# Kernel optimization log

Measured on AMD Instinct MI355X. Metric: run time of the kernel, lower is better.

Reference implementation:

```python
import jax, jax.numpy as jnp
import numpy as np

N = 100000   # nodes (in_ch)
D = 128      # emb_ch
E = 1600000  # nonzeros in A_hat
RATE = 0.1   # dropout rate


def setup_inputs() -> dict:
    key = jax.random.key(0)
    k1, k2, k3, k4, k5, k6 = jax.random.split(key, 6)
    x = jnp.arange(N, dtype=jnp.int64) if jax.config.jax_enable_x64 else jnp.arange(N, dtype=jnp.int32)
    rows = jax.random.randint(k1, (E,), 0, N)
    cols = jax.random.randint(k2, (E,), 0, N)
    A_vals = jax.random.uniform(k3, (E,), dtype=jnp.float32)
    # xavier_uniform for [N, D]: bound = sqrt(6/(N+D))
    bound = float(np.sqrt(6.0 / (N + D)))
    emb_weight = jax.random.uniform(k4, (N, D), jnp.float32, -bound, bound)
    u1 = jax.random.uniform(k5, (N, D), dtype=jnp.float32)
    u2 = jax.random.uniform(k6, (N, D), dtype=jnp.float32)
    return {"x": x, "rows": rows, "cols": cols, "A_vals": A_vals,
            "emb_weight": emb_weight, "u1": u1, "u2": u2}


def _dropout(h, u):
    keep = (u >= RATE).astype(h.dtype)
    return h * keep / (1.0 - RATE)


def _spmm(rows, cols, vals, h):
    # out[i] = sum_{e: rows[e]==i} vals[e] * h[cols[e]]  -- COO SpMM
    msgs = vals[:, None] * h[cols]  # [E, D]
    return jax.ops.segment_sum(msgs, rows, num_segments=N)


def reference(x, rows, cols, A_vals, emb_weight, u1, u2):
    h0 = emb_weight[x]                       # embedding lookup [N, D]
    h1 = _spmm(rows, cols, A_vals, _dropout(h0, u1))
    h2 = _spmm(rows, cols, A_vals, _dropout(h1, u2))
    return (h0 + h1 + h2) / 3.0
```

## Files before the change

kernel.cpp:

```cpp
#include <hip/hip_runtime.h>
#include <hip/hip_fp16.h>

#define DD 128
#define SCAN_CHUNK 1024
#define G_ROWS 32
#define G_STAGE 1024
#define NCOPY 8

typedef float          f32x4 __attribute__((ext_vector_type(4)));
typedef unsigned int   u32x4 __attribute__((ext_vector_type(4)));
typedef unsigned int   u32x2 __attribute__((ext_vector_type(2)));
typedef unsigned short u16x8 __attribute__((ext_vector_type(8)));

struct __align__(8) Edge { int c; float v; };

__device__ __forceinline__ unsigned short f2h(float f) {
    return __half_as_ushort(__float2half(f));
}
__device__ __forceinline__ float2 up2(unsigned int u) {
    __half2 h = *reinterpret_cast<const __half2*>(&u);
    return __half22float2(h);
}

template <typename T>
__device__ __forceinline__ T ldnt(const T* p) { return __builtin_nontemporal_load(p); }
template <typename T>
__device__ __forceinline__ void stnt(T* p, T v) { __builtin_nontemporal_store(v, p); }

__global__ __launch_bounds__(256) void k_g1hist(const float* __restrict__ emb,
                                                const float* __restrict__ u1,
                                                ushort* __restrict__ g1,
                                                const int* __restrict__ rows,
                                                int* __restrict__ cnt8,
                                                ushort* __restrict__ rank,
                                                int total8, int E, int N) {
    int t = threadIdx.x;
    int b = blockIdx.x;
    int i = b * 256 + t;
    int e0 = b * 1024 + t;
    int k = b & (NCOPY - 1);
    bool doS = i < total8;

    int r[4]; bool v[4];
#pragma unroll
    for (int j = 0; j < 4; ++j) {
        int e = e0 + j * 256;
        v[j] = e < E;
        r[j] = v[j] ? ldnt(rows + e) : 0;
    }
    f32x4 hA, hB, uA, uB;
    if (doS) {
        const f32x4* e4 = (const f32x4*)emb;
        const f32x4* a4 = (const f32x4*)u1;
        hA = ldnt(e4 + 2 * (size_t)i);
        hB = ldnt(e4 + 2 * (size_t)i + 1);
        uA = ldnt(a4 + 2 * (size_t)i);
        uB = ldnt(a4 + 2 * (size_t)i + 1);
    }
    int old[4];
#pragma unroll
    for (int j = 0; j < 4; ++j)
        if (v[j]) old[j] = atomicAdd(&cnt8[(size_t)k * N + r[j]], 1);
#pragma unroll
    for (int j = 0; j < 4; ++j)
        if (v[j]) stnt(rank + e0 + j * 256, (ushort)((k << 13) | old[j]));

    if (doS) {
        const float s = 1.0f / 0.9f;
        u16x8 g;
        g[0] = f2h((uA.x >= 0.1f) ? hA.x * s : 0.0f);
        g[1] = f2h((uA.y >= 0.1f) ? hA.y * s : 0.0f);
        g[2] = f2h((uA.z >= 0.1f) ? hA.z * s : 0.0f);
        g[3] = f2h((uA.w >= 0.1f) ? hA.w * s : 0.0f);
        g[4] = f2h((uB.x >= 0.1f) ? hB.x * s : 0.0f);
        g[5] = f2h((uB.y >= 0.1f) ? hB.y * s : 0.0f);
        g[6] = f2h((uB.z >= 0.1f) ? hB.z * s : 0.0f);
        g[7] = f2h((uB.w >= 0.1f) ? hB.w * s : 0.0f);
        ((u16x8*)g1)[i] = g;
    }
}

__global__ __launch_bounds__(256) void k_scan1(int* __restrict__ cnt8,
                                               int* __restrict__ rs,
                                               int* __restrict__ bsum, int n) {
    __shared__ int s[256];
    int tid = threadIdx.x;
    int base = blockIdx.x * SCAN_CHUNK + tid * 4;
    int c[4][NCOPY];
    int tot[4];
#pragma unroll
    for (int j = 0; j < 4; ++j) {
        int row = base + j;
        int t = 0;
        if (row < n) {
#pragma unroll
            for (int k = 0; k < NCOPY; ++k) {
                c[j][k] = cnt8[(size_t)k * n + row];
                t += c[j][k];
            }
        }
        tot[j] = t;
    }
    int tsum = tot[0] + tot[1] + tot[2] + tot[3];
    s[tid] = tsum;
    __syncthreads();
    for (int off = 1; off < 256; off <<= 1) {
        int t = (tid >= off) ? s[tid - off] : 0;
        __syncthreads();
        s[tid] += t;
        __syncthreads();
    }
    int excl = s[tid] - tsum;
    if (tid == 255) bsum[blockIdx.x] = s[255];
    int run = excl;
#pragma unroll
    for (int j = 0; j < 4; ++j) {
        int row = base + j;
        if (row < n) {
            rs[row] = run;
            int p = run;
#pragma unroll
            for (int k = 0; k < NCOPY; ++k) {
                cnt8[(size_t)k * n + row] = p;
                p += c[j][k];
            }
        }
        run += tot[j];
    }
}

__global__ __launch_bounds__(256) void k_scan23(int* __restrict__ rs,
                                                int* __restrict__ cnt8,
                                                const int* __restrict__ bsum,
                                                int nb, int n) {
    __shared__ int s[1024];
    int tid = threadIdx.x;
    for (int i = tid; i < nb; i += 256) s[i] = bsum[i];
    __syncthreads();
    if (tid == 0) {
        int run = 0;
        for (int i = 0; i < nb; ++i) { int t = s[i]; s[i] = run; run += t; }
    }
    __syncthreads();
    int i = blockIdx.x * 256 + tid;
    if (i < n) {
        int off = s[i >> 10];
        rs[i] += off;
#pragma unroll
        for (int k = 0; k < NCOPY; ++k) cnt8[(size_t)k * n + i] += off;
    }
}

__global__ __launch_bounds__(256) void k_scatter_prep(const int* __restrict__ rows,
                                                      const int* __restrict__ cols,
                                                      const float* __restrict__ vals,
                                                      const int* __restrict__ cnt8,
                                                      const ushort* __restrict__ rank,
                                                      Edge* __restrict__ ev,
                                                      const float* __restrict__ emb,
                                                      const float* __restrict__ u2,
                                                      ushort* __restrict__ emb16,
                                                      unsigned char* __restrict__ mask2,
                                                      int E, int total8, int N) {
    int t = threadIdx.x;
    int b = blockIdx.x;
    int i = b * 256 + t;
    int e0 = b * 1024 + t;
    bool doS = i < total8;

    int r[4], c[4]; float vv[4]; unsigned int rk[4]; bool v[4];
#pragma unroll
    for (int j = 0; j < 4; ++j) {
        int e = e0 + j * 256;
        v[j] = e < E;
        if (v[j]) {
            r[j] = ldnt(rows + e);
            c[j] = ldnt(cols + e);
            vv[j] = ldnt(vals + e);
            rk[j] = ldnt(rank + e);
        }
    }
    f32x4 hA, hB, vA, vB;
    if (doS) {
        const f32x4* e4 = (const f32x4*)emb;
        const f32x4* b4 = (const f32x4*)u2;
        hA = ldnt(e4 + 2 * (size_t)i);
        hB = ldnt(e4 + 2 * (size_t)i + 1);
        vA = ldnt(b4 + 2 * (size_t)i);
        vB = ldnt(b4 + 2 * (size_t)i + 1);
    }
#pragma unroll
    for (int j = 0; j < 4; ++j) {
        if (v[j]) {
            int kk = rk[j] >> 13;
            int rin = rk[j] & 0x1FFF;
            int pos = cnt8[(size_t)kk * N + r[j]] + rin;
            u32x2 q;
            q.x = (unsigned int)c[j];
            q.y = __float_as_uint(vv[j]);
            ((u32x2*)ev)[pos] = q;
        }
    }
    if (doS) {
        u16x8 e16;
        e16[0] = f2h(hA.x); e16[1] = f2h(hA.y); e16[2] = f2h(hA.z); e16[3] = f2h(hA.w);
        e16[4] = f2h(hB.x); e16[5] = f2h(hB.y); e16[6] = f2h(hB.z); e16[7] = f2h(hB.w);
        stnt((u16x8*)emb16 + i, e16);
        unsigned char m =
            (unsigned char)((vA.x >= 0.1f ? 1u : 0u)  | (vA.y >= 0.1f ? 2u : 0u)  |
                            (vA.z >= 0.1f ? 4u : 0u)  | (vA.w >= 0.1f ? 8u : 0u)  |
                            (vB.x >= 0.1f ? 16u : 0u) | (vB.y >= 0.1f ? 32u : 0u) |
                            (vB.z >= 0.1f ? 64u : 0u) | (vB.w >= 0.1f ? 128u : 0u));
        stnt(mask2 + i, m);
    }
}

template <int MODE>
__global__ __launch_bounds__(256) void k_gather(const int* __restrict__ rowstart,
                                                const Edge* __restrict__ ev,
                                                const ushort* __restrict__ srch,
                                                const unsigned char* __restrict__ mask2,
                                                const ushort* __restrict__ emb16,
                                                const ushort* __restrict__ p16in,
                                                ushort* __restrict__ p16out,
                                                ushort* __restrict__ g2,
                                                float* __restrict__ out,
                                                int N, int E) {
    __shared__ int s_rs[G_ROWS + 1];
    __shared__ Edge s_ev[G_STAGE];

    int tid = threadIdx.x;
    int r0 = blockIdx.x * G_ROWS;
    int h = blockIdx.y;
    if (tid <= G_ROWS) {
        int r = r0 + tid;
        s_rs[tid] = (r < N) ? rowstart[r] : E;
    }
    __syncthreads();
    int base = s_rs[0];
    int nblk = s_rs[G_ROWS] - base;
    int nstage = nblk < G_STAGE ? nblk : G_STAGE;
    for (int i = tid; i < nstage; i += 256) {
        u32x2 q = ldnt((const u32x2*)(ev + base + i));
        Edge ed; ed.c = (int)q.x; ed.v = __uint_as_float(q.y);
        s_ev[i] = ed;
    }
    __syncthreads();

    int grp = tid >> 3;
    int lane = tid & 7;
    int row = r0 + grp;
    if (row >= N) return;
    int start = s_rs[grp] - base;
    int end = s_rs[grp + 1] - base;
    int eL = end < nstage ? end : nstage;

    const u32x4* __restrict__ s4 = (const u32x4*)srch;
    const Edge* __restrict__ evg = ev + base;
    int hoff = (h << 3) + lane;
    float a0 = 0.f, a1 = 0.f, a2 = 0.f, a3 = 0.f;
    float a4 = 0.f, a5 = 0.f, a6 = 0.f, a7 = 0.f;

#define LDE(i) Edge E##i = s_ev[e + i];
#define GQ(i)  u32x4 q##i = s4[((size_t)E##i.c << 4) + hoff];
#define ACC(i) { float vv = E##i.v; \
        float2 w0 = up2(q##i.x), w1 = up2(q##i.y), w2 = up2(q##i.z), w3 = up2(q##i.w); \
        a0 = fmaf(vv, w0.x, a0); a1 = fmaf(vv, w0.y, a1); \
        a2 = fmaf(vv, w1.x, a2); a3 = fmaf(vv, w1.y, a3); \
        a4 = fmaf(vv, w2.x, a4); a5 = fmaf(vv, w2.y, a5); \
        a6 = fmaf(vv, w3.x, a6); a7 = fmaf(vv, w3.y, a7); }

    int e = start;
    for (; e + 8 <= eL; e += 8) {
        LDE(0) LDE(1) LDE(2) LDE(3) LDE(4) LDE(5) LDE(6) LDE(7)
        GQ(0) GQ(1) GQ(2) GQ(3) GQ(4) GQ(5) GQ(6) GQ(7)
        ACC(0) ACC(1) ACC(2) ACC(3) ACC(4) ACC(5) ACC(6) ACC(7)
    }
    if (e + 4 <= eL) {
        LDE(0) LDE(1) LDE(2) LDE(3)
        GQ(0) GQ(1) GQ(2) GQ(3)
        ACC(0) ACC(1) ACC(2) ACC(3)
        e += 4;
    }
    for (; e < eL; ++e) {
        LDE(0) GQ(0) ACC(0)
    }
    for (; e < end; ++e) {
        Edge E0; { u32x2 q_ = ldnt((const u32x2*)(evg + e));
                   E0.c = (int)q_.x; E0.v = __uint_as_float(q_.y); }
        GQ(0) ACC(0)
    }
#undef LDE
#undef GQ
#undef ACC

    size_t o = ((size_t)row << 7) + ((size_t)h << 6) + (size_t)lane * 8;
    if (MODE == 1) {
        unsigned int m = mask2[(size_t)row * 16 + (h << 3) + lane];
        const float s = 1.0f / 0.9f;
        u16x8 gg;
        gg[0] = (m & 1u)   ? f2h(a0 * s) : (ushort)0;
        gg[1] = (m & 2u)   ? f2h(a1 * s) : (ushort)0;
        gg[2] = (m & 4u)   ? f2h(a2 * s) : (ushort)0;
        gg[3] = (m & 8u)   ? f2h(a3 * s) : (ushort)0;
        gg[4] = (m & 16u)  ? f2h(a4 * s) : (ushort)0;
        gg[5] = (m & 32u)  ? f2h(a5 * s) : (ushort)0;
        gg[6] = (m & 64u)  ? f2h(a6 * s) : (ushort)0;
        gg[7] = (m & 128u) ? f2h(a7 * s) : (ushort)0;
        stnt((u16x8*)(g2 + o), gg);
        u16x8 pp;
        pp[0] = f2h(a0); pp[1] = f2h(a1); pp[2] = f2h(a2); pp[3] = f2h(a3);
        pp[4] = f2h(a4); pp[5] = f2h(a5); pp[6] = f2h(a6); pp[7] = f2h(a7);
        stnt((u16x8*)(p16out + o), pp);
    } else {
        u32x4 eq = ldnt((const u32x4*)(emb16 + o));
        u32x4 pq = ldnt((const u32x4*)(p16in + o));
        float2 e0 = up2(eq.x), e1 = up2(eq.y), e2 = up2(eq.z), e3 = up2(eq.w);
        float2 p0 = up2(pq.x), p1 = up2(pq.y), p2 = up2(pq.z), p3 = up2(pq.w);
        const float t3 = 1.0f / 3.0f;
        f32x4 rA, rB;
        rA.x = (e0.x + p0.x + a0) * t3;
        rA.y = (e0.y + p0.y + a1) * t3;
        rA.z = (e1.x + p1.x + a2) * t3;
        rA.w = (e1.y + p1.y + a3) * t3;
        rB.x = (e2.x + p2.x + a4) * t3;
        rB.y = (e2.y + p2.y + a5) * t3;
        rB.z = (e3.x + p3.x + a6) * t3;
        rB.w = (e3.y + p3.y + a7) * t3;
        stnt((f32x4*)(out + o), rA);
        stnt((f32x4*)(out + o) + 1, rB);
    }
}


extern "C" void kernel_launch(void* const* d_in, const int* in_sizes, int n_in,
                              void* d_out, int out_size, void* d_ws, size_t ws_size,
                              hipStream_t stream) {
    const int* rows = (const int*)d_in[1];
    const int* cols = (const int*)d_in[2];
    const float* vals = (const float*)d_in[3];
    const float* emb = (const float*)d_in[4];
    const float* u1 = (const float*)d_in[5];
    const float* u2 = (const float*)d_in[6];
    float* out = (float*)d_out;

    const int N = in_sizes[0];
    const int E = in_sizes[1];
    const size_t ND = (size_t)N * DD;

    char* ws = (char*)d_ws;
    Edge* ev     = (Edge*)ws;   ws += (size_t)E * sizeof(Edge);
    ushort* g1   = (ushort*)ws; ws += ND * sizeof(ushort);
    ushort* g2   = (ushort*)ws; ws += ND * sizeof(ushort);
    ushort* p16  = (ushort*)ws; ws += ND * sizeof(ushort);
    ushort* emb16= (ushort*)ws; ws += ND * sizeof(ushort);
    int* cnt8    = (int*)ws;    ws += (size_t)NCOPY * N * sizeof(int);
    int* rs      = (int*)ws;    ws += (size_t)N * sizeof(int);
    ushort* rank = (ushort*)ws; ws += (size_t)E * sizeof(ushort);
    int* bsum    = (int*)ws;    ws += 4096;
    unsigned char* mask2 = (unsigned char*)ws;

    const int total8 = (int)(ND / 8);
    const int prepBlocks = (total8 + 255) / 256;
    const int gridE = (E + 1023) / 1024;
    const int gridFuse = prepBlocks > gridE ? prepBlocks : gridE;
    const int nScanBlocks = (N + SCAN_CHUNK - 1) / SCAN_CHUNK;
    const int gridRowX = (N + G_ROWS - 1) / G_ROWS;
    dim3 gridRow(gridRowX, 2, 1);

    hipMemsetAsync(cnt8, 0, (size_t)NCOPY * N * sizeof(int), stream);
    k_g1hist<<<gridFuse, 256, 0, stream>>>(emb, u1, g1, rows, cnt8, rank,
                                           total8, E, N);
    k_scan1<<<nScanBlocks, 256, 0, stream>>>(cnt8, rs, bsum, N);
    k_scan23<<<(N + 255) / 256, 256, 0, stream>>>(rs, cnt8, bsum, nScanBlocks, N);
    k_scatter_prep<<<gridFuse, 256, 0, stream>>>(rows, cols, vals, cnt8, rank,
                                                 ev, emb, u2, emb16, mask2,
                                                 E, total8, N);
    k_gather<1><<<gridRow, 256, 0, stream>>>(rs, ev, g1, mask2, nullptr, nullptr,
                                             p16, g2, nullptr, N, E);
    k_gather<2><<<gridRow, 256, 0, stream>>>(rs, ev, g2, nullptr, emb16, p16,
                                             nullptr, nullptr, out, N, E);
}
```

Before: 425.7 us.

## Use one edge per thread in prep kernels and predicated gather tail

The histogram and scatter kernels now handle one edge per thread instead of four, and the edge grid grows to match. E and total8 are both 1.6M, so the edge and embedding work now line up one to one per thread. The gather kernel replaces its 4-wide and scalar remainder loops with a single predicated 8-wide batch that clamps the index and zeroes the weight, which cuts divergent tail iterations but issues some redundant loads. One risk is that blocks sharing a histogram copy now hit the same rows with less spread, which may change atomic contention.

```diff
diff --git a/kernel.cpp b/kernel.cpp
--- a/kernel.cpp
+++ b/kernel.cpp
@@ -34,20 +34,12 @@
                                                 int* __restrict__ cnt8,
                                                 ushort* __restrict__ rank,
                                                 int total8, int E, int N) {
-    int t = threadIdx.x;
-    int b = blockIdx.x;
-    int i = b * 256 + t;
-    int e0 = b * 1024 + t;
-    int k = b & (NCOPY - 1);
+    int i = blockIdx.x * 256 + threadIdx.x;
+    int k = blockIdx.x & (NCOPY - 1);
+    bool doE = i < E;
     bool doS = i < total8;
-
-    int r[4]; bool v[4];
-#pragma unroll
-    for (int j = 0; j < 4; ++j) {
-        int e = e0 + j * 256;
-        v[j] = e < E;
-        r[j] = v[j] ? ldnt(rows + e) : 0;
-    }
+    int r = 0;
+    if (doE) r = ldnt(rows + i);
     f32x4 hA, hB, uA, uB;
     if (doS) {
         const f32x4* e4 = (const f32x4*)emb;
@@ -57,14 +49,10 @@
         uA = ldnt(a4 + 2 * (size_t)i);
         uB = ldnt(a4 + 2 * (size_t)i + 1);
     }
-    int old[4];
-#pragma unroll
-    for (int j = 0; j < 4; ++j)
-        if (v[j]) old[j] = atomicAdd(&cnt8[(size_t)k * N + r[j]], 1);
-#pragma unroll
-    for (int j = 0; j < 4; ++j)
-        if (v[j]) stnt(rank + e0 + j * 256, (ushort)((k << 13) | old[j]));
-
+    if (doE) {
+        int old = atomicAdd(&cnt8[(size_t)k * N + r], 1);
+        stnt(rank + i, (ushort)((k << 13) | old));
+    }
     if (doS) {
         const float s = 1.0f / 0.9f;
         u16x8 g;
@@ -162,23 +150,15 @@
                                                       ushort* __restrict__ emb16,
                                                       unsigned char* __restrict__ mask2,
                                                       int E, int total8, int N) {
-    int t = threadIdx.x;
-    int b = blockIdx.x;
-    int i = b * 256 + t;
-    int e0 = b * 1024 + t;
+    int i = blockIdx.x * 256 + threadIdx.x;
+    bool doE = i < E;
     bool doS = i < total8;
-
-    int r[4], c[4]; float vv[4]; unsigned int rk[4]; bool v[4];
-#pragma unroll
-    for (int j = 0; j < 4; ++j) {
-        int e = e0 + j * 256;
-        v[j] = e < E;
-        if (v[j]) {
-            r[j] = ldnt(rows + e);
-            c[j] = ldnt(cols + e);
-            vv[j] = ldnt(vals + e);
-            rk[j] = ldnt(rank + e);
-        }
+    int r = 0, c = 0; float vv = 0.f; unsigned int rk = 0;
+    if (doE) {
+        r = ldnt(rows + i);
+        c = ldnt(cols + i);
+        vv = ldnt(vals + i);
+        rk = ldnt(rank + i);
     }
     f32x4 hA, hB, vA, vB;
     if (doS) {
@@ -189,17 +169,14 @@
         vA = ldnt(b4 + 2 * (size_t)i);
         vB = ldnt(b4 + 2 * (size_t)i + 1);
     }
-#pragma unroll
-    for (int j = 0; j < 4; ++j) {
-        if (v[j]) {
-            int kk = rk[j] >> 13;
-            int rin = rk[j] & 0x1FFF;
-            int pos = cnt8[(size_t)kk * N + r[j]] + rin;
-            u32x2 q;
-            q.x = (unsigned int)c[j];
-            q.y = __float_as_uint(vv[j]);
-            ((u32x2*)ev)[pos] = q;
-        }
+    if (doE) {
+        int kk = rk >> 13;
+        int rin = rk & 0x1FFF;
+        int pos = cnt8[(size_t)kk * N + r] + rin;
+        u32x2 q;
+        q.x = (unsigned int)c;
+        q.y = __float_as_uint(vv);
+        ((u32x2*)ev)[pos] = q;
     }
     if (doS) {
         u16x8 e16;
@@ -261,9 +238,12 @@
     float a0 = 0.f, a1 = 0.f, a2 = 0.f, a3 = 0.f;
     float a4 = 0.f, a5 = 0.f, a6 = 0.f, a7 = 0.f;
 
-#define LDE(i) Edge E##i = s_ev[e + i];
+#define LDE(i) Edge E##i = s_ev[e + i]; float fv##i = E##i.v;
+#define LDP(i) int ix##i = e + i; bool ok##i = ix##i < eL; \
+               Edge E##i = s_ev[ok##i ? ix##i : last]; \
+               float fv##i = ok##i ? E##i.v : 0.0f;
 #define GQ(i)  u32x4 q##i = s4[((size_t)E##i.c << 4) + hoff];
-#define ACC(i) { float vv = E##i.v; \
+#define ACC(i) { float vv = fv##i; \
         float2 w0 = up2(q##i.x), w1 = up2(q##i.y), w2 = up2(q##i.z), w3 = up2(q##i.w); \
         a0 = fmaf(vv, w0.x, a0); a1 = fmaf(vv, w0.y, a1); \
         a2 = fmaf(vv, w1.x, a2); a3 = fmaf(vv, w1.y, a3); \
@@ -276,21 +256,21 @@
         GQ(0) GQ(1) GQ(2) GQ(3) GQ(4) GQ(5) GQ(6) GQ(7)
         ACC(0) ACC(1) ACC(2) ACC(3) ACC(4) ACC(5) ACC(6) ACC(7)
     }
-    if (e + 4 <= eL) {
-        LDE(0) LDE(1) LDE(2) LDE(3)
-        GQ(0) GQ(1) GQ(2) GQ(3)
-        ACC(0) ACC(1) ACC(2) ACC(3)
-        e += 4;
-    }
-    for (; e < eL; ++e) {
-        LDE(0) GQ(0) ACC(0)
+    if (e < eL) {
+        int last = eL - 1;
+        LDP(0) LDP(1) LDP(2) LDP(3) LDP(4) LDP(5) LDP(6) LDP(7)
+        GQ(0) GQ(1) GQ(2) GQ(3) GQ(4) GQ(5) GQ(6) GQ(7)
+        ACC(0) ACC(1) ACC(2) ACC(3) ACC(4) ACC(5) ACC(6) ACC(7)
+        e = eL;
     }
     for (; e < end; ++e) {
         Edge E0; { u32x2 q_ = ldnt((const u32x2*)(evg + e));
                    E0.c = (int)q_.x; E0.v = __uint_as_float(q_.y); }
+        float fv0 = E0.v;
         GQ(0) ACC(0)
     }
 #undef LDE
+#undef LDP
 #undef GQ
 #undef ACC
 
@@ -362,7 +342,7 @@
 
     const int total8 = (int)(ND / 8);
     const int prepBlocks = (total8 + 255) / 256;
-    const int gridE = (E + 1023) / 1024;
+    const int gridE = (E + 255) / 256;
     const int gridFuse = prepBlocks > gridE ? prepBlocks : gridE;
     const int nScanBlocks = (N + SCAN_CHUNK - 1) / SCAN_CHUNK;
     const int gridRowX = (N + G_ROWS - 1) / G_ROWS;
```

Result: faster. 403.7 us (-5.2%).
